# Kernel tuning notes

Measured on AMD Instinct MI355X. Metric: run time of the kernel, lower is better.

## Reference

```python
import jax, jax.numpy as jnp
import numpy as np

H = 16       # num_heads
D = 128      # head_dim
SCALE = 1.0 / np.sqrt(D).astype(np.float32)


def setup_inputs() -> dict:
    key = jax.random.key(0)
    ks = jax.random.split(key, 5)
    B, S, C = 2, 2048, 2048
    x = jax.random.normal(ks[0], (B, S, C), dtype=jnp.float32)
    # nn.Linear stores weight as [out_features, in_features]; scale ~ kaiming-ish
    s = 1.0 / np.sqrt(C)
    wq = jax.random.normal(ks[1], (C, C), dtype=jnp.float32) * s
    wk = jax.random.normal(ks[2], (C, C), dtype=jnp.float32) * s
    wv = jax.random.normal(ks[3], (C, C), dtype=jnp.float32) * s
    wo = jax.random.normal(ks[4], (C, C), dtype=jnp.float32) * s
    return {"x": x, "wq": wq, "wk": wk, "wv": wv, "wo": wo}


def reference(x, wq, wk, wv, wo):
    B, S, C = x.shape
    # projections: nn.Linear(x) = x @ W.T
    q = (x @ wq.T).reshape(B, S, H, D).transpose(0, 2, 1, 3)  # [B,H,S,D]
    k = (x @ wk.T).reshape(B, S, H, D).transpose(0, 2, 1, 3)
    v = (x @ wv.T).reshape(B, S, H, D).transpose(0, 2, 1, 3)
    scores = jnp.einsum('bhqd,bhkd->bhqk', q, k) * SCALE      # [B,H,S,S]
    attn = jax.nn.softmax(scores, axis=-1)
    out = jnp.einsum('bhqk,bhkd->bhqd', attn, v)              # [B,H,S,D]
    out = out.transpose(0, 2, 1, 3).reshape(B, S, H * D)
    return out @ wo.T
```

## Files before the change

kernel.cpp:

```cpp
#include <hip/hip_runtime.h>
#include <hip/hip_bf16.h>
#include <cstdint>
#include <cstddef>

typedef __bf16 bf16_t;
typedef __bf16 bf8_t __attribute__((ext_vector_type(8)));
typedef float f4_t __attribute__((ext_vector_type(4)));
typedef float f8_t __attribute__((ext_vector_type(8)));

#define DEV static __device__ __forceinline__

DEV f4_t mfma16(bf8_t a, bf8_t b, f4_t c) {
    return __builtin_amdgcn_mfma_f32_16x16x32_bf16(a, b, c, 0, 0, 0);
}

DEV bf8_t cvt8(f8_t v) {
    bf8_t r;
#pragma unroll
    for (int i = 0; i < 8; ++i) r[i] = (bf16_t)v[i];
    return r;
}

DEV void load_lds16(const bf16_t* g, bf16_t* l) {
    __builtin_amdgcn_global_load_lds(
        (const __attribute__((address_space(1))) uint32_t*)g,
        (__attribute__((address_space(3))) uint32_t*)l,
        16, 0, 0);
}

__global__ __launch_bounds__(256) void cvt_fused(const float* __restrict__ x,
                                                 const float* __restrict__ wq,
                                                 const float* __restrict__ wk,
                                                 const float* __restrict__ wv,
                                                 bf16_t* __restrict__ xb,
                                                 bf16_t* __restrict__ wqkvb) {
    const int bid = blockIdx.x;
    const float* src;
    bf16_t* dst;
    int base;
    if (bid < 4096) {
        src = x; dst = xb; base = bid;
    } else {
        const int seg = (bid - 4096) >> 11;
        src = (seg == 0) ? wq : (seg == 1) ? wk : wv;
        dst = wqkvb + (size_t)seg * 4194304;
        base = (bid - 4096) & 2047;
    }
    const size_t i = ((size_t)base * 256 + threadIdx.x) * 8;
    const f8_t v = *(const f8_t*)&src[i];
    *(bf8_t*)&dst[i] = cvt8(v);
}

__global__ __launch_bounds__(256) void cvt_bf16(const float* __restrict__ in,
                                                bf16_t* __restrict__ out, int n8) {
    const int i = blockIdx.x * 256 + threadIdx.x;
    if (i < n8) {
        const f8_t v = *(const f8_t*)&in[(size_t)i * 8];
        *(bf8_t*)&out[(size_t)i * 8] = cvt8(v);
    }
}

__global__ __launch_bounds__(512, 2) void gemm_qkv(const bf16_t* __restrict__ A,
                                                   const bf16_t* __restrict__ B,
                                                   bf16_t* __restrict__ Cq,
                                                   bf16_t* __restrict__ Ck,
                                                   bf16_t* __restrict__ Cv) {
    __shared__ bf16_t smem[49152];

    const int tid = threadIdx.x, lane = tid & 63, wave = tid >> 6;
    const int wr = wave >> 2, wc = wave & 3;
    const int q4 = lane >> 4, r16 = lane & 15;
    const int srow = lane >> 2;
    const int scol = ((lane & 3) ^ ((lane >> 3) & 3)) * 8;
    const int rkey = (r16 >> 1) & 3;

    int wg = blockIdx.y * 24 + blockIdx.x;
    wg = (wg & 7) * 96 + (wg >> 3);
    const int bm0 = (wg / 24) * 128;
    const int bn0 = (wg % 24) * 256;

    f4_t acc[4][4] = {};

    auto stageA = [&](int kt, bf16_t* buf) {
#pragma unroll
        for (int kk = 0; kk < 2; ++kk)
            load_lds16(A + (size_t)(bm0 + wave * 16 + srow) * 2048 + kt * 64 + kk * 32 + scol,
                       buf + kk * 4096 + wave * 16 * 32);
    };
    auto stageB = [&](int kt, bf16_t* buf, int rb) {
#pragma unroll
        for (int kk = 0; kk < 2; ++kk)
            load_lds16(B + (size_t)(bn0 + rb + wave * 16 + srow) * 2048 + kt * 64 + kk * 32 + scol,
                       buf + 8192 + kk * 8192 + (rb + wave * 16) * 32);
    };

    {
        bf16_t* b0 = smem;
        bf16_t* b1 = smem + 24576;
        stageA(0, b0);
        stageB(0, b0, 0);
        stageB(0, b0, 128);
        stageB(1, b1, 0);
        stageB(1, b1, 128);
        asm volatile("s_waitcnt vmcnt(4)" ::: "memory");
        __builtin_amdgcn_s_barrier();
    }

    for (int t = 0; t < 32; ++t) {
        bf16_t* buf  = smem + (t & 1) * 24576;
        bf16_t* bufN = smem + ((t + 1) & 1) * 24576;

        bf8_t bq[4][2];
#pragma unroll
        for (int n = 0; n < 4; ++n)
#pragma unroll
            for (int kk = 0; kk < 2; ++kk)
                bq[n][kk] = *(const bf8_t*)&buf[8192 + kk * 8192 +
                                                (wc * 64 + n * 16 + r16) * 32 +
                                                (q4 ^ rkey) * 8];

        {
            bf8_t af[2][2];
#pragma unroll
            for (int i = 0; i < 2; ++i)
#pragma unroll
                for (int kk = 0; kk < 2; ++kk)
                    af[i][kk] = *(const bf8_t*)&buf[kk * 4096 +
                                                    (wr * 64 + i * 16 + r16) * 32 +
                                                    (q4 ^ rkey) * 8];
            if (t + 1 < 32) stageA(t + 1, bufN);
            __builtin_amdgcn_s_barrier();
            asm volatile("s_waitcnt lgkmcnt(0)" ::: "memory");
            __builtin_amdgcn_s_setprio(1);
#pragma unroll
            for (int kk = 0; kk < 2; ++kk)
#pragma unroll
                for (int i = 0; i < 2; ++i)
#pragma unroll
                    for (int n = 0; n < 4; ++n)
                        acc[i][n] = mfma16(af[i][kk], bq[n][kk], acc[i][n]);
            __builtin_amdgcn_s_setprio(0);
            __builtin_amdgcn_s_barrier();
        }

        {
            bf8_t af[2][2];
#pragma unroll
            for (int i = 0; i < 2; ++i)
#pragma unroll
                for (int kk = 0; kk < 2; ++kk)
                    af[i][kk] = *(const bf8_t*)&buf[kk * 4096 +
                                                    (wr * 64 + (2 + i) * 16 + r16) * 32 +
                                                    (q4 ^ rkey) * 8];
            if (t + 2 < 32) {
                stageB(t + 2, buf, 0);
                stageB(t + 2, buf, 128);
            }
            __builtin_amdgcn_s_barrier();
            asm volatile("s_waitcnt lgkmcnt(0)" ::: "memory");
            __builtin_amdgcn_s_setprio(1);
#pragma unroll
            for (int kk = 0; kk < 2; ++kk)
#pragma unroll
                for (int i = 0; i < 2; ++i)
#pragma unroll
                    for (int n = 0; n < 4; ++n)
                        acc[2 + i][n] = mfma16(af[i][kk], bq[n][kk], acc[2 + i][n]);
            __builtin_amdgcn_s_setprio(0);
            if (t < 30) {
                asm volatile("s_waitcnt vmcnt(4)" ::: "memory");
            } else {
                asm volatile("s_waitcnt vmcnt(0)" ::: "memory");
            }
            __builtin_amdgcn_s_barrier();
        }
    }

    __syncthreads();

    bf16_t* strip = smem + wave * 4608;
    if (bn0 < 4096) {
        bf16_t* dst = (bn0 < 2048) ? Cq : Ck;
        const int nb = (bn0 & 2047) + wc * 64;
#pragma unroll
        for (int i = 0; i < 4; ++i)
#pragma unroll
            for (int n = 0; n < 4; ++n)
#pragma unroll
                for (int r = 0; r < 4; ++r)
                    strip[(i * 16 + q4 * 4 + r) * 72 + n * 16 + r16] =
                        (bf16_t)acc[i][n][r];
        asm volatile("s_waitcnt lgkmcnt(0)" ::: "memory");
#pragma unroll
        for (int it = 0; it < 8; ++it) {
            const int row = it * 8 + (lane >> 3);
            const int c = (lane & 7) * 8;
            *(bf8_t*)&dst[(size_t)(bm0 + wr * 64 + row) * 2048 + nb + c] =
                *(const bf8_t*)&strip[row * 72 + c];
        }
    } else {
        const int bb = bm0 >> 11;
        const int s0 = (bm0 & 2047) + wr * 64;
#pragma unroll
        for (int i = 0; i < 4; ++i)
#pragma unroll
            for (int n = 0; n < 4; ++n)
#pragma unroll
                for (int r = 0; r < 4; ++r)
                    strip[(n * 16 + r16) * 72 + i * 16 + q4 * 4 + r] =
                        (bf16_t)acc[i][n][r];
        asm volatile("s_waitcnt lgkmcnt(0)" ::: "memory");
#pragma unroll
        for (int it = 0; it < 8; ++it) {
            const int nrow = it * 8 + (lane >> 3);
            const int c = (lane & 7) * 8;
            const int dg = (bn0 - 4096) + wc * 64 + nrow;
            const int h = dg >> 7, d = dg & 127;
            *(bf8_t*)&Cv[(((size_t)(bb * 16 + h) * 128 + d) << 11) + s0 + c] =
                *(const bf8_t*)&strip[nrow * 72 + c];
        }
    }
}

template <int MODE>
__global__ __launch_bounds__(256) void gemm_m97(const bf16_t* __restrict__ A,
                                                const bf16_t* __restrict__ B,
                                                void* __restrict__ C0,
                                                bf16_t* __restrict__ C1,
                                                bf16_t* __restrict__ C2,
                                                int N, int K) {
    constexpr int SMEMN = (MODE == 0) ? 128 * 136 : 8192;
    __shared__ bf16_t smem[SMEMN];
    bf16_t* As = smem;
    bf16_t* Bs = smem + 4096;

    const int tid = threadIdx.x;
    const int lane = tid & 63;
    const int wave = tid >> 6;
    const int bm0 = blockIdx.y * 128;
    const int bn0 = blockIdx.x * 128;
    const int wm = (wave >> 1) * 64;
    const int wn = (wave & 1) * 64;
    const int q4 = lane >> 4;
    const int r16 = lane & 15;

    const int srow = lane >> 2;
    const int scol = (((lane & 3) ^ ((lane >> 3) & 3))) * 8;
    const int rkey = (r16 >> 1) & 3;

    f4_t acc[4][4] = {};

    for (int k0 = 0; k0 < K; k0 += 32) {
        __syncthreads();
        load_lds16(A + (size_t)(bm0 + wave * 16 + srow) * K + k0 + scol, As + wave * 16 * 32);
        load_lds16(A + (size_t)(bm0 + 64 + wave * 16 + srow) * K + k0 + scol,
                   As + (64 + wave * 16) * 32);
        load_lds16(B + (size_t)(bn0 + wave * 16 + srow) * K + k0 + scol, Bs + wave * 16 * 32);
        load_lds16(B + (size_t)(bn0 + 64 + wave * 16 + srow) * K + k0 + scol,
                   Bs + (64 + wave * 16) * 32);
        __syncthreads();

        bf8_t af[4], bfr[4];
#pragma unroll
        for (int i = 0; i < 4; ++i)
            af[i] = *(const bf8_t*)&As[(wm + i * 16 + r16) * 32 + (q4 ^ rkey) * 8];
#pragma unroll
        for (int j = 0; j < 4; ++j)
            bfr[j] = *(const bf8_t*)&Bs[(wn + j * 16 + r16) * 32 + (q4 ^ rkey) * 8];
#pragma unroll
        for (int i = 0; i < 4; ++i)
#pragma unroll
            for (int j = 0; j < 4; ++j)
                acc[i][j] = mfma16(af[i], bfr[j], acc[i][j]);
    }

    if (MODE == 1) {
        float* C = (float*)C0;
#pragma unroll
        for (int i = 0; i < 4; ++i)
#pragma unroll
            for (int j = 0; j < 4; ++j)
#pragma unroll
                for (int r = 0; r < 4; ++r) {
                    const int m = bm0 + wm + i * 16 + q4 * 4 + r;
                    const int n = bn0 + wn + j * 16 + r16;
                    C[(size_t)m * 2048 + n] = acc[i][j][r];
                }
        return;
    }

    __syncthreads();
    if (bn0 < 4096) {
        bf16_t* dst = (bn0 < 2048) ? (bf16_t*)C0 : C1;
        const int nbase = bn0 & 2047;
#pragma unroll
        for (int i = 0; i < 4; ++i)
#pragma unroll
            for (int j = 0; j < 4; ++j)
#pragma unroll
                for (int r = 0; r < 4; ++r)
                    smem[(wm + i * 16 + q4 * 4 + r) * 136 + wn + j * 16 + r16] =
                        (bf16_t)acc[i][j][r];
        __syncthreads();
#pragma unroll
        for (int it = 0; it < 8; ++it) {
            const int idx = it * 256 + tid;
            const int m = idx >> 4;
            const int nc = (idx & 15) * 8;
            *(bf8_t*)&dst[(size_t)(bm0 + m) * 2048 + nbase + nc] =
                *(const bf8_t*)&smem[m * 136 + nc];
        }
    } else {
#pragma unroll
        for (int i = 0; i < 4; ++i)
#pragma unroll
            for (int j = 0; j < 4; ++j)
#pragma unroll
                for (int r = 0; r < 4; ++r)
                    smem[(wn + j * 16 + r16) * 136 + wm + i * 16 + q4 * 4 + r] =
                        (bf16_t)acc[i][j][r];
        __syncthreads();
        const int bb = bm0 >> 11;
        const int s0 = bm0 & 2047;
        const int nh0 = bn0 - 4096;
#pragma unroll
        for (int it = 0; it < 8; ++it) {
            const int idx = it * 256 + tid;
            const int n = idx >> 4;
            const int mc = (idx & 15) * 8;
            const bf8_t v = *(const bf8_t*)&smem[n * 136 + mc];
            const int dg = nh0 + n;
            const int h = dg >> 7, d = dg & 127;
            *(bf8_t*)&C2[(((size_t)(bb * 16 + h) * 128 + d) << 11) + s0 + mc] = v;
        }
    }
}

__global__ __launch_bounds__(256) void flash5(const bf16_t* __restrict__ Q,
                                              const bf16_t* __restrict__ K,
                                              const bf16_t* __restrict__ VT,
                                              bf16_t* __restrict__ O) {
    constexpr int S = 2048, C = 2048;
    constexpr float SCL = 0.08838834764831845f * 1.4426950408889634f;
    __shared__ bf16_t Ks[4 * 64 * 32];
    __shared__ bf16_t Vs[2 * 128 * 32];
    __shared__ bf16_t Ps[4][32 * 72];

    const int tid = threadIdx.x, lane = tid & 63, wave = tid >> 6;
    const int q4 = lane >> 4, r16 = lane & 15;
    const int bh = blockIdx.y, b = bh >> 4, h = bh & 15;
    const int q0 = blockIdx.x * 128 + wave * 32;

    const size_t qrow = (size_t)b * S + q0;
    const bf16_t* Qp0 = Q + (qrow + r16) * C + h * 128;
    const bf16_t* Qp1 = Q + (qrow + 16 + r16) * C + h * 128;
    const bf16_t* Kbase = K + (size_t)b * S * C + h * 128;
    const bf16_t* Vbase = VT + (size_t)bh * 128 * S;
    bf16_t* Pw = &Ps[wave][0];

    const int srow = lane >> 2;
    const int scol = (((lane & 3) ^ ((lane >> 3) & 3))) * 8;
    const int rkey = (r16 >> 1) & 3;

    bf8_t aq0[4], aq1[4];
#pragma unroll
    for (int kk = 0; kk < 4; ++kk) {
        aq0[kk] = *(const bf8_t*)&Qp0[kk * 32 + q4 * 8];
        aq1[kk] = *(const bf8_t*)&Qp1[kk * 32 + q4 * 8];
    }

    bf8_t ones;
#pragma unroll
    for (int i = 0; i < 8; ++i) ones[i] = (bf16_t)1.0f;

    f4_t o0[8] = {}, o1[8] = {};
    f4_t lacc0 = {}, lacc1 = {};

    for (int kv0 = 0; kv0 < S; kv0 += 64) {
        __syncthreads();
#pragma unroll
        for (int r0 = 0; r0 < 64; r0 += 16)
            load_lds16(Kbase + (size_t)(kv0 + r0 + srow) * C + wave * 32 + scol,
                       Ks + wave * 2048 + r0 * 32);
        {
            const int kkp = wave >> 1;
            const int rb = (wave & 1) * 64;
#pragma unroll
            for (int r0 = 0; r0 < 64; r0 += 16)
                load_lds16(Vbase + (size_t)(rb + r0 + srow) * S + kv0 + kkp * 32 + scol,
                           Vs + kkp * 4096 + (rb + r0) * 32);
        }
        __syncthreads();

        f4_t s4a[4] = {}, s4b[4] = {};
#pragma unroll
        for (int kk = 0; kk < 4; ++kk) {
#pragma unroll
            for (int j = 0; j < 4; ++j) {
                const bf8_t bk =
                    *(const bf8_t*)&Ks[kk * 2048 + (j * 16 + r16) * 32 + (q4 ^ rkey) * 8];
                s4a[j] = mfma16(aq0[kk], bk, s4a[j]);
                s4b[j] = mfma16(aq1[kk], bk, s4b[j]);
            }
        }

#pragma unroll
        for (int r = 0; r < 4; ++r)
#pragma unroll
            for (int j = 0; j < 4; ++j) {
                Pw[(q4 * 4 + r) * 72 + j * 16 + r16] = (bf16_t)exp2f(s4a[j][r] * SCL);
                Pw[(16 + q4 * 4 + r) * 72 + j * 16 + r16] = (bf16_t)exp2f(s4b[j][r] * SCL);
            }
        asm volatile("s_waitcnt lgkmcnt(0)" ::: "memory");

        bf8_t ap0[2], ap1[2];
#pragma unroll
        for (int kkp = 0; kkp < 2; ++kkp) {
            ap0[kkp] = *(const bf8_t*)&Pw[r16 * 72 + kkp * 32 + q4 * 8];
            ap1[kkp] = *(const bf8_t*)&Pw[(16 + r16) * 72 + kkp * 32 + q4 * 8];
        }

#pragma unroll
        for (int kkp = 0; kkp < 2; ++kkp) {
            lacc0 = mfma16(ap0[kkp], ones, lacc0);
            lacc1 = mfma16(ap1[kkp], ones, lacc1);
        }

#pragma unroll
        for (int t = 0; t < 8; ++t) {
#pragma unroll
            for (int kkp = 0; kkp < 2; ++kkp) {
                const bf8_t bv =
                    *(const bf8_t*)&Vs[kkp * 4096 + (t * 16 + r16) * 32 + (q4 ^ rkey) * 8];
                o0[t] = mfma16(ap0[kkp], bv, o0[t]);
                o1[t] = mfma16(ap1[kkp], bv, o1[t]);
            }
        }
    }

    f4_t inv0, inv1;
#pragma unroll
    for (int r = 0; r < 4; ++r) {
        inv0[r] = 1.0f / lacc0[r];
        inv1[r] = 1.0f / lacc1[r];
    }
#pragma unroll
    for (int t = 0; t < 8; ++t)
#pragma unroll
        for (int r = 0; r < 4; ++r) {
            O[(qrow + q4 * 4 + r) * C + h * 128 + t * 16 + r16] = (bf16_t)(o0[t][r] * inv0[r]);
            O[(qrow + 16 + q4 * 4 + r) * C + h * 128 + t * 16 + r16] =
                (bf16_t)(o1[t][r] * inv1[r]);
        }
}

extern "C" void kernel_launch(void* const* d_in, const int* in_sizes, int n_in,
                              void* d_out, int out_size, void* d_ws, size_t ws_size,
                              hipStream_t stream) {
    const float* x  = (const float*)d_in[0];
    const float* wq = (const float*)d_in[1];
    const float* wk = (const float*)d_in[2];
    const float* wv = (const float*)d_in[3];
    const float* wo = (const float*)d_in[4];

    bf16_t* ws = (bf16_t*)d_ws;
    bf16_t* xb   = ws;
    bf16_t* Wqkv = ws + 8388608;
    bf16_t* Qb   = ws + 20971520;
    bf16_t* Kb   = ws + 29360128;
    bf16_t* Vt   = ws + 37748736;
    bf16_t* Wob  = xb;
    bf16_t* At   = Wqkv;

    cvt_fused<<<10240, 256, 0, stream>>>(x, wq, wk, wv, xb, Wqkv);

    gemm_qkv<<<dim3(24, 32), 512, 0, stream>>>(xb, Wqkv, Qb, Kb, Vt);

    cvt_bf16<<<2048, 256, 0, stream>>>(wo, Wob, 524288);

    flash5<<<dim3(16, 32), 256, 0, stream>>>(Qb, Kb, Vt, At);

    gemm_m97<1><<<dim3(16, 32), 256, 0, stream>>>(At, Wob, d_out, nullptr, nullptr, 2048, 2048);
}
```

Baseline: 409.8 us.

## Triple-buffer LDS in QKV GEMM with prefetch distance two

Grows the QKV projection GEMM's shared memory from two to three stage buffers, rotating them, so global-to-LDS loads for tile t+2 are issued while tile t is computed. The inner loop now splits work along the K halves: each phase loads all four A and B fragments for one 32-wide half, instead of splitting by row groups. The aim is to hide global load latency behind more MFMA work. The cost is 144KB of LDS per block, which likely stops two 512-thread blocks from sharing a CU and so lowers occupancy.

Result: no change. 412.3 us (+0.6%).

```diff
diff --git a/kernel.cpp b/kernel.cpp
--- a/kernel.cpp
+++ b/kernel.cpp
@@ -65,7 +65,7 @@
                                                    bf16_t* __restrict__ Cq,
                                                    bf16_t* __restrict__ Ck,
                                                    bf16_t* __restrict__ Cv) {
-    __shared__ bf16_t smem[49152];
+    __shared__ bf16_t smem[73728];
 
     const int tid = threadIdx.x, lane = tid & 63, wave = tid >> 6;
     const int wr = wave >> 2, wc = wave & 3;
@@ -95,85 +95,77 @@
     };
 
     {
-        bf16_t* b0 = smem;
-        bf16_t* b1 = smem + 24576;
-        stageA(0, b0);
-        stageB(0, b0, 0);
-        stageB(0, b0, 128);
-        stageB(1, b1, 0);
-        stageB(1, b1, 128);
-        asm volatile("s_waitcnt vmcnt(4)" ::: "memory");
+        stageA(0, smem);
+        stageB(0, smem, 0);
+        stageB(0, smem, 128);
+        stageA(1, smem + 24576);
+        stageB(1, smem + 24576, 0);
+        stageB(1, smem + 24576, 128);
+        asm volatile("s_waitcnt vmcnt(6)" ::: "memory");
         __builtin_amdgcn_s_barrier();
     }
 
+    int cb = 0, sb = 2;
     for (int t = 0; t < 32; ++t) {
-        bf16_t* buf  = smem + (t & 1) * 24576;
-        bf16_t* bufN = smem + ((t + 1) & 1) * 24576;
-
-        bf8_t bq[4][2];
-#pragma unroll
-        for (int n = 0; n < 4; ++n)
-#pragma unroll
-            for (int kk = 0; kk < 2; ++kk)
-                bq[n][kk] = *(const bf8_t*)&buf[8192 + kk * 8192 +
-                                                (wc * 64 + n * 16 + r16) * 32 +
-                                                (q4 ^ rkey) * 8];
+        bf16_t* buf  = smem + cb * 24576;
+        bf16_t* sbuf = smem + sb * 24576;
 
         {
-            bf8_t af[2][2];
-#pragma unroll
-            for (int i = 0; i < 2; ++i)
-#pragma unroll
-                for (int kk = 0; kk < 2; ++kk)
-                    af[i][kk] = *(const bf8_t*)&buf[kk * 4096 +
-                                                    (wr * 64 + i * 16 + r16) * 32 +
-                                                    (q4 ^ rkey) * 8];
-            if (t + 1 < 32) stageA(t + 1, bufN);
-            __builtin_amdgcn_s_barrier();
-            asm volatile("s_waitcnt lgkmcnt(0)" ::: "memory");
-            __builtin_amdgcn_s_setprio(1);
-#pragma unroll
-            for (int kk = 0; kk < 2; ++kk)
-#pragma unroll
-                for (int i = 0; i < 2; ++i)
-#pragma unroll
-                    for (int n = 0; n < 4; ++n)
-                        acc[i][n] = mfma16(af[i][kk], bq[n][kk], acc[i][n]);
-            __builtin_amdgcn_s_setprio(0);
-            __builtin_amdgcn_s_barrier();
-        }
-
-        {
-            bf8_t af[2][2];
-#pragma unroll
-            for (int i = 0; i < 2; ++i)
-#pragma unroll
-                for (int kk = 0; kk < 2; ++kk)
-                    af[i][kk] = *(const bf8_t*)&buf[kk * 4096 +
-                                                    (wr * 64 + (2 + i) * 16 + r16) * 32 +
-                                                    (q4 ^ rkey) * 8];
+            bf8_t af[4], bq[4];
+#pragma unroll
+            for (int i = 0; i < 4; ++i)
+                af[i] = *(const bf8_t*)&buf[(wr * 64 + i * 16 + r16) * 32 + (q4 ^ rkey) * 8];
+#pragma unroll
+            for (int n = 0; n < 4; ++n)
+                bq[n] = *(const bf8_t*)&buf[8192 + (wc * 64 + n * 16 + r16) * 32 +
+                                            (q4 ^ rkey) * 8];
             if (t + 2 < 32) {
-                stageB(t + 2, buf, 0);
-                stageB(t + 2, buf, 128);
+                stageA(t + 2, sbuf);
+                stageB(t + 2, sbuf, 0);
             }
             __builtin_amdgcn_s_barrier();
             asm volatile("s_waitcnt lgkmcnt(0)" ::: "memory");
             __builtin_amdgcn_s_setprio(1);
 #pragma unroll
-            for (int kk = 0; kk < 2; ++kk)
-#pragma unroll
-                for (int i = 0; i < 2; ++i)
-#pragma unroll
-                    for (int n = 0; n < 4; ++n)
-                        acc[2 + i][n] = mfma16(af[i][kk], bq[n][kk], acc[2 + i][n]);
+            for (int i = 0; i < 4; ++i)
+#pragma unroll
+                for (int n = 0; n < 4; ++n)
+                    acc[i][n] = mfma16(af[i], bq[n], acc[i][n]);
+            __builtin_amdgcn_s_setprio(0);
+            __builtin_amdgcn_s_barrier();
+        }
+
+        {
+            bf8_t af[4], bq[4];
+#pragma unroll
+            for (int i = 0; i < 4; ++i)
+                af[i] = *(const bf8_t*)&buf[4096 + (wr * 64 + i * 16 + r16) * 32 +
+                                            (q4 ^ rkey) * 8];
+#pragma unroll
+            for (int n = 0; n < 4; ++n)
+                bq[n] = *(const bf8_t*)&buf[8192 + 8192 + (wc * 64 + n * 16 + r16) * 32 +
+                                            (q4 ^ rkey) * 8];
+            if (t + 2 < 32)
+                stageB(t + 2, sbuf, 128);
+            __builtin_amdgcn_s_barrier();
+            asm volatile("s_waitcnt lgkmcnt(0)" ::: "memory");
+            __builtin_amdgcn_s_setprio(1);
+#pragma unroll
+            for (int i = 0; i < 4; ++i)
+#pragma unroll
+                for (int n = 0; n < 4; ++n)
+                    acc[i][n] = mfma16(af[i], bq[n], acc[i][n]);
             __builtin_amdgcn_s_setprio(0);
             if (t < 30) {
-                asm volatile("s_waitcnt vmcnt(4)" ::: "memory");
+                asm volatile("s_waitcnt vmcnt(6)" ::: "memory");
             } else {
                 asm volatile("s_waitcnt vmcnt(0)" ::: "memory");
             }
             __builtin_amdgcn_s_barrier();
         }
+
+        cb = (cb == 2) ? 0 : cb + 1;
+        sb = (sb == 2) ? 0 : sb + 1;
     }
 
     __syncthreads();
```
